# Performance work log

Hardware: AMD Instinct MI355X
Metric: run time of the kernel (lower is better)

## Reference

```python
import jax, jax.numpy as jnp
import numpy as np

N_NODES = 100000
N_EDGES = 1200000
NODE_IN = 64
EDGE_IN = 32
HIDDEN = 64


def _glorot(key, shape):
    fan_in, fan_out = shape[0], shape[1]
    s = jnp.sqrt(2.0 / (fan_in + fan_out))
    return jax.random.normal(key, shape, dtype=jnp.float32) * s


def setup_inputs() -> dict:
    key = jax.random.key(0)
    ks = jax.random.split(key, 16)
    inp = {
        "x": jax.random.normal(ks[0], (N_NODES, NODE_IN), dtype=jnp.float32),
        "edge_index": jax.random.randint(ks[1], (2, N_EDGES), 0, N_NODES, dtype=jnp.int64),
        "edge_attr": jax.random.normal(ks[2], (N_EDGES, EDGE_IN), dtype=jnp.float32),
        # SAGE layer 0 (in=NODE_IN -> HIDDEN): lin_l (neighbors, has bias), lin_r (root)
        "w_l0": _glorot(ks[3], (NODE_IN, HIDDEN)),
        "w_r0": _glorot(ks[4], (NODE_IN, HIDDEN)),
        "b0": jnp.zeros((HIDDEN,), jnp.float32),
        "ln_g0": jnp.ones((HIDDEN,), jnp.float32),
        "ln_b0": jnp.zeros((HIDDEN,), jnp.float32),
        # SAGE layer 1 (HIDDEN -> HIDDEN)
        "w_l1": _glorot(ks[5], (HIDDEN, HIDDEN)),
        "w_r1": _glorot(ks[6], (HIDDEN, HIDDEN)),
        "b1": jnp.zeros((HIDDEN,), jnp.float32),
        "ln_g1": jnp.ones((HIDDEN,), jnp.float32),
        "ln_b1": jnp.zeros((HIDDEN,), jnp.float32),
        # Edge classifier MLP: in_dim = 3*HIDDEN + EDGE_IN = 224
        "cw1": _glorot(ks[7], (3 * HIDDEN + EDGE_IN, HIDDEN)),
        "cb1": jnp.zeros((HIDDEN,), jnp.float32),
        "cw2": _glorot(ks[8], (HIDDEN, HIDDEN // 2)),
        "cb2": jnp.zeros((HIDDEN // 2,), jnp.float32),
        "cw3": _glorot(ks[9], (HIDDEN // 2, 1)),
        "cb3": jnp.zeros((1,), jnp.float32),
    }
    return inp


def _sage_conv(x, src, dst, w_l, w_r, b):
    # mean-aggregate source features at destination nodes (PyG SAGEConv, aggr='mean')
    n = x.shape[0]
    msg = x[src]  # [E, F] gather
    agg = jax.ops.segment_sum(msg, dst, num_segments=n)
    cnt = jax.ops.segment_sum(jnp.ones((src.shape[0], 1), x.dtype), dst, num_segments=n)
    mean = agg / jnp.maximum(cnt, 1.0)
    return mean @ w_l + x @ w_r + b


def _layer_norm(x, g, b, eps=1e-5):
    mu = jnp.mean(x, axis=-1, keepdims=True)
    var = jnp.var(x, axis=-1, keepdims=True)
    return (x - mu) * jax.lax.rsqrt(var + eps) * g + b


def reference(x, edge_index, edge_attr,
              w_l0, w_r0, b0, ln_g0, ln_b0,
              w_l1, w_r1, b1, ln_g1, ln_b1,
              cw1, cb1, cw2, cb2, cw3, cb3):
    src, dst = edge_index[0], edge_index[1]
    # Encoder (eval mode: dropout is identity)
    h = jax.nn.relu(_layer_norm(_sage_conv(x, src, dst, w_l0, w_r0, b0), ln_g0, ln_b0))
    z = jax.nn.relu(_layer_norm(_sage_conv(h, src, dst, w_l1, w_r1, b1), ln_g1, ln_b1))
    # Edge classifier: gather-concat-MLP
    z_src = z[src]
    z_dst = z[dst]
    edge_repr = jnp.concatenate([z_src, z_dst, z_src * z_dst, edge_attr], axis=-1)
    h1 = jax.nn.relu(edge_repr @ cw1 + cb1)
    h2 = jax.nn.relu(h1 @ cw2 + cb2)
    logits = (h2 @ cw3 + cb3).squeeze(-1)  # [E]
    return logits
```

## Files before the change

kernel.cpp:

```cpp
#include <hip/hip_runtime.h>
#include <hip/hip_bf16.h>

#define N_NODES 100000
#define N_EDGES 1200000

typedef __attribute__((ext_vector_type(8))) short bfrag;
typedef __attribute__((ext_vector_type(4))) float ffrag;

union FragU { uint4 v; uint32_t u[4]; bfrag f; };

__device__ __forceinline__ float rl_f(float v, int k) {
  return __int_as_float(__builtin_amdgcn_readlane(__float_as_int(v), k));
}
__device__ __forceinline__ int rl_i(int v, int k) {
  return __builtin_amdgcn_readlane(v, k);
}
__device__ __forceinline__ ushort bfbits(float a) {
  union { __hip_bfloat16 h; ushort u; } c; c.h = __float2bfloat16(a); return c.u;
}
__device__ __forceinline__ uint32_t pkbf(float a, float b) {
  union { __hip_bfloat162 h; uint32_t u; } c;
  c.h = __float22bfloat162_rn(float2{a, b}); return c.u;
}
__device__ __forceinline__ uint32_t mul2bf(uint32_t a, uint32_t b) {
  union { uint32_t u; __hip_bfloat162 h; } x, y, r;
  x.u = a; y.u = b; r.h = __hmul2(x.h, y.h); return r.u;
}
__device__ __forceinline__ float bflo(uint32_t u) { return __int_as_float(u << 16); }
__device__ __forceinline__ float bfhi(uint32_t u) { return __int_as_float(u & 0xffff0000u); }


__global__ void cvt_k(const float* __restrict__ x, ushort* __restrict__ xb, int n2) {
  int i = blockIdx.x * blockDim.x + threadIdx.x;
  if (i < n2) {
    float2 v = ((const float2*)x)[i];
    ((uint32_t*)xb)[i] = pkbf(v.x, v.y);
  }
}


__global__ void hist_k(const int* __restrict__ ei, int* __restrict__ deg, int E) {
  int e = blockIdx.x * blockDim.x + threadIdx.x;
  if (e < E) atomicAdd(&deg[ei[E + e]], 1);
}

__global__ __launch_bounds__(1024) void scan1_k(const int* __restrict__ deg,
                                                int* __restrict__ off,
                                                int* __restrict__ bsum, int n) {
  __shared__ int wpart[16];
  __shared__ int wpre[16];
  int tid = threadIdx.x, lane = tid & 63, wid = tid >> 6;
  int i = blockIdx.x * 1024 + tid;
  int v = (i < n) ? deg[i] : 0;
  int x = v;
  #pragma unroll
  for (int o = 1; o < 64; o <<= 1) {
    int y = __shfl_up(x, o);
    if (lane >= o) x += y;
  }
  if (lane == 63) wpart[wid] = x;
  __syncthreads();
  if (tid == 0) {
    int run = 0;
    #pragma unroll
    for (int w = 0; w < 16; w++) { int t = wpart[w]; wpre[w] = run; run += t; }
    bsum[blockIdx.x] = run;
  }
  __syncthreads();
  if (i < n) off[i] = x - v + wpre[wid];
}

__global__ void scan2_k(const int* __restrict__ bsum, int* __restrict__ bpre,
                        int* __restrict__ off, int nb, int n) {
  if (threadIdx.x == 0) {
    int run = 0;
    for (int b = 0; b < nb; b++) { int t = bsum[b]; bpre[b] = run; run += t; }
    off[n] = run;
  }
}

__global__ __launch_bounds__(1024) void scan3_k(int* __restrict__ off, int* __restrict__ pos,
                                                const int* __restrict__ bpre, int n) {
  int i = blockIdx.x * 1024 + threadIdx.x;
  if (i < n) {
    int o = off[i] + bpre[blockIdx.x];
    off[i] = o;
    pos[i] = o;
  }
}

__global__ void fill_k(const int* __restrict__ ei, int* __restrict__ pos,
                       int* __restrict__ csr, int E) {
  int e = blockIdx.x * blockDim.x + threadIdx.x;
  if (e < E) {
    int d = ei[E + e];
    int p = atomicAdd(&pos[d], 1);
    csr[p] = ei[e];
  }
}


__global__ __launch_bounds__(256) void agg_k(
    const ushort* __restrict__ Xb, const int* __restrict__ off, const int* __restrict__ csr,
    ushort* __restrict__ aggout, int n) {
  int lane = threadIdx.x & 63;
  int half = lane >> 5, f2 = lane & 31;
  int wave = blockIdx.x * 4 + (threadIdx.x >> 6);
  int nw = gridDim.x * 4;
  for (int i = wave; i < n; i += nw) {
    int s0 = off[i], s1 = off[i + 1];
    float a0 = 0.f, a1 = 0.f;
    for (int base = s0; base < s1; base += 64) {
      int rem = s1 - base;
      int cnt = rem < 64 ? rem : 64;
      int myidx = (lane < cnt) ? csr[base + lane] : 0;
      int j = 0;
      for (; j + 8 <= cnt; j += 8) {
        uint32_t us[4];
        #pragma unroll
        for (int p = 0; p < 4; p++) {
          int i0 = rl_i(myidx, j + 2 * p), i1 = rl_i(myidx, j + 2 * p + 1);
          int sel = half ? i1 : i0;
          us[p] = ((const uint32_t*)Xb)[(size_t)sel * 32 + f2];
        }
        #pragma unroll
        for (int p = 0; p < 4; p++) { a0 += bflo(us[p]); a1 += bfhi(us[p]); }
      }
      for (; j + 2 <= cnt; j += 2) {
        int i0 = rl_i(myidx, j), i1 = rl_i(myidx, j + 1);
        int sel = half ? i1 : i0;
        uint32_t u = ((const uint32_t*)Xb)[(size_t)sel * 32 + f2];
        a0 += bflo(u); a1 += bfhi(u);
      }
      if (j < cnt) {
        int i0 = rl_i(myidx, j);
        uint32_t u = ((const uint32_t*)Xb)[(size_t)i0 * 32 + f2];
        if (half == 0) { a0 += bflo(u); a1 += bfhi(u); }
      }
    }
    a0 += __shfl_xor(a0, 32);
    a1 += __shfl_xor(a1, 32);
    int d = s1 - s0;
    float rdeg = 1.f / fmaxf((float)d, 1.f);
    if (half == 0)
      ((uint32_t*)aggout)[(size_t)i * 32 + f2] = pkbf(a0 * rdeg, a1 * rdeg);
  }
}


__global__ __launch_bounds__(256) void node_k(
    const ushort* __restrict__ agg, const ushort* __restrict__ selfb,
    const float* __restrict__ wl, const float* __restrict__ wr,
    const float* __restrict__ bias, const float* __restrict__ g, const float* __restrict__ lb,
    ushort* __restrict__ outb, int n) {
  __shared__ ushort wt[64 * 128];
  const int tid = threadIdx.x;
  for (int i = tid; i < 8192; i += 256) {
    int k = i >> 6, nn = i & 63;
    float v = (k < 64) ? wl[k * 64 + nn] : wr[(k - 64) * 64 + nn];
    wt[nn * 128 + (((k >> 3) ^ (nn & 7)) * 8) + (k & 7)] = bfbits(v);
  }
  __syncthreads();
  const int lane = tid & 63, wid = tid >> 6;
  const int ln = lane & 15, q = lane >> 4;
  float bias_n[4], g_n[4], lb_n[4];
  #pragma unroll
  for (int nt = 0; nt < 4; nt++) {
    bias_n[nt] = bias[nt * 16 + ln];
    g_n[nt] = g[nt * 16 + ln];
    lb_n[nt] = lb[nt * 16 + ln];
  }
  const int ntiles = (n + 15) >> 4;
  for (int t = blockIdx.x * 4 + wid; t < ntiles; t += gridDim.x * 4) {
    int node = t * 16 + ln;
    int nc = node < n ? node : n - 1;
    FragU afr[4];
    #pragma unroll
    for (int kk = 0; kk < 2; kk++) {
      afr[kk].v     = ((const uint4*)agg)[(size_t)nc * 8 + kk * 4 + q];
      afr[2 + kk].v = ((const uint4*)selfb)[(size_t)nc * 8 + kk * 4 + q];
    }
    ffrag acc[4];
    #pragma unroll
    for (int nt = 0; nt < 4; nt++) acc[nt] = ffrag{0.f, 0.f, 0.f, 0.f};
    #pragma unroll
    for (int kk = 0; kk < 4; kk++) {
      bfrag a = afr[kk].f;
      #pragma unroll
      for (int nt = 0; nt < 4; nt++) {
        int nn = nt * 16 + ln;
        int b = kk * 4 + q;
        const bfrag* bp = (const bfrag*)&wt[nn * 128 + ((b ^ (nn & 7)) * 8)];
        acc[nt] = __builtin_amdgcn_mfma_f32_16x16x32_bf16(a, *bp, acc[nt], 0, 0, 0);
      }
    }
    #pragma unroll
    for (int r = 0; r < 4; r++) {
      int m = t * 16 + q * 4 + r;
      float o[4];
      #pragma unroll
      for (int nt = 0; nt < 4; nt++) o[nt] = acc[nt][r] + bias_n[nt];
      float s = (o[0] + o[1]) + (o[2] + o[3]);
      #pragma unroll
      for (int mm = 1; mm < 16; mm <<= 1) s += __shfl_xor(s, mm);
      float mu = s * (1.f / 64.f);
      float v2 = 0.f;
      #pragma unroll
      for (int nt = 0; nt < 4; nt++) { float d2 = o[nt] - mu; v2 += d2 * d2; }
      #pragma unroll
      for (int mm = 1; mm < 16; mm <<= 1) v2 += __shfl_xor(v2, mm);
      float rs = rsqrtf(v2 * (1.f / 64.f) + 1e-5f);
      if (m < n) {
        #pragma unroll
        for (int nt = 0; nt < 4; nt++) {
          float y = fmaxf((o[nt] - mu) * rs * g_n[nt] + lb_n[nt], 0.f);
          outb[(size_t)m * 64 + nt * 16 + ln] = bfbits(y);
        }
      }
    }
  }
}


__global__ __launch_bounds__(256) void edge_mfma_k(
    const int* __restrict__ ei, const float* __restrict__ ea,
    const ushort* __restrict__ zb,
    const float* __restrict__ cw1, const float* __restrict__ cb1,
    const float* __restrict__ cw2, const float* __restrict__ cb2,
    const float* __restrict__ cw3, const float* __restrict__ cb3,
    float* __restrict__ out, int E) {
  __shared__ ushort wt1[64 * 256];
  __shared__ ushort h1b[4][16 * 64];
  const int tid = threadIdx.x;

  for (int i = tid; i < 224 * 64; i += 256) {
    int k = i >> 6, n = i & 63;
    int blk = k >> 3;
    wt1[n * 256 + ((blk ^ (n & 7)) * 8) + (k & 7)] = bfbits(cw1[i]);
  }
  __syncthreads();

  const int lane = tid & 63, wid = tid >> 6;
  const int ln = lane & 15, q = lane >> 4;

  float cb1v[4];
  #pragma unroll
  for (int t = 0; t < 4; t++) cb1v[t] = cb1[t * 16 + ln];
  float cb2a = cb2[ln], cb2b = cb2[16 + ln];
  float w3a = cw3[ln], w3b = cw3[16 + ln];
  float cb3v = cb3[0];

  FragU w2f[2][2];
  #pragma unroll
  for (int t2 = 0; t2 < 2; t2++) {
    #pragma unroll
    for (int kk = 0; kk < 2; kk++) {
      #pragma unroll
      for (int p = 0; p < 4; p++) {
        int k = kk * 32 + q * 8 + p * 2;
        int n = t2 * 16 + ln;
        w2f[t2][kk].u[p] = pkbf(cw2[k * 32 + n], cw2[(k + 1) * 32 + n]);
      }
    }
  }

  ushort* hb = h1b[wid];
  const int ntiles = E >> 4;
  for (int t = blockIdx.x * 4 + wid; t < ntiles; t += gridDim.x * 4) {
    int e = t * 16 + ln;
    int s = ei[e], d = ei[E + e];

    FragU afr[7];
    #pragma unroll
    for (int kk = 0; kk < 2; kk++) {
      afr[kk].v     = ((const uint4*)zb)[(size_t)s * 8 + kk * 4 + q];
      afr[2 + kk].v = ((const uint4*)zb)[(size_t)d * 8 + kk * 4 + q];
    }
    #pragma unroll
    for (int kk = 0; kk < 2; kk++) {
      #pragma unroll
      for (int p = 0; p < 4; p++)
        afr[4 + kk].u[p] = mul2bf(afr[kk].u[p], afr[2 + kk].u[p]);
    }
    {
      float4 lo = ((const float4*)ea)[(size_t)e * 8 + q * 2];
      float4 hi = ((const float4*)ea)[(size_t)e * 8 + q * 2 + 1];
      afr[6].u[0] = pkbf(lo.x, lo.y); afr[6].u[1] = pkbf(lo.z, lo.w);
      afr[6].u[2] = pkbf(hi.x, hi.y); afr[6].u[3] = pkbf(hi.z, hi.w);
    }

    ffrag acc1[4];
    #pragma unroll
    for (int tt = 0; tt < 4; tt++) acc1[tt] = ffrag{0.f, 0.f, 0.f, 0.f};

    #pragma unroll
    for (int kk = 0; kk < 7; kk++) {
      bfrag a = afr[kk].f;
      #pragma unroll
      for (int tt = 0; tt < 4; tt++) {
        int n = tt * 16 + ln;
        int b = kk * 4 + q;
        const bfrag* bp = (const bfrag*)&wt1[n * 256 + ((b ^ (n & 7)) * 8)];
        acc1[tt] = __builtin_amdgcn_mfma_f32_16x16x32_bf16(a, *bp, acc1[tt], 0, 0, 0);
      }
    }

    #pragma unroll
    for (int tt = 0; tt < 4; tt++) {
      #pragma unroll
      for (int r = 0; r < 4; r++) {
        int m = q * 4 + r;
        int col = tt * 16 + ln;
        float v = fmaxf(acc1[tt][r] + cb1v[tt], 0.f);
        hb[m * 64 + (((col >> 3) ^ (m & 7)) * 8) + (col & 7)] = bfbits(v);
      }
    }

    ffrag acc2[2];
    acc2[0] = ffrag{0.f, 0.f, 0.f, 0.f};
    acc2[1] = ffrag{0.f, 0.f, 0.f, 0.f};
    #pragma unroll
    for (int kk = 0; kk < 2; kk++) {
      int b = kk * 4 + q;
      const bfrag* ap = (const bfrag*)&hb[ln * 64 + ((b ^ (ln & 7)) * 8)];
      bfrag a2 = *ap;
      acc2[0] = __builtin_amdgcn_mfma_f32_16x16x32_bf16(a2, w2f[0][kk].f, acc2[0], 0, 0, 0);
      acc2[1] = __builtin_amdgcn_mfma_f32_16x16x32_bf16(a2, w2f[1][kk].f, acc2[1], 0, 0, 0);
    }

    float p0, p1, p2, p3;
    {
      p0 = fmaxf(acc2[0][0] + cb2a, 0.f) * w3a + fmaxf(acc2[1][0] + cb2b, 0.f) * w3b;
      p1 = fmaxf(acc2[0][1] + cb2a, 0.f) * w3a + fmaxf(acc2[1][1] + cb2b, 0.f) * w3b;
      p2 = fmaxf(acc2[0][2] + cb2a, 0.f) * w3a + fmaxf(acc2[1][2] + cb2b, 0.f) * w3b;
      p3 = fmaxf(acc2[0][3] + cb2a, 0.f) * w3a + fmaxf(acc2[1][3] + cb2b, 0.f) * w3b;
    }
    #pragma unroll
    for (int o = 1; o < 16; o <<= 1) {
      p0 += __shfl_xor(p0, o);
      p1 += __shfl_xor(p1, o);
      p2 += __shfl_xor(p2, o);
      p3 += __shfl_xor(p3, o);
    }
    float keep = (ln == 0) ? p0 : (ln == 1) ? p1 : (ln == 2) ? p2 : p3;
    if (ln < 4) out[t * 16 + q * 4 + ln] = keep + cb3v;
  }
}


extern "C" void kernel_launch(void* const* d_in, const int* in_sizes, int n_in,
                              void* d_out, int out_size, void* d_ws, size_t ws_size,
                              hipStream_t stream) {
  const float* x   = (const float*)d_in[0];
  const int*   ei  = (const int*)d_in[1];
  const float* ea  = (const float*)d_in[2];
  const float* wl0 = (const float*)d_in[3];
  const float* wr0 = (const float*)d_in[4];
  const float* b0  = (const float*)d_in[5];
  const float* g0  = (const float*)d_in[6];
  const float* lb0 = (const float*)d_in[7];
  const float* wl1 = (const float*)d_in[8];
  const float* wr1 = (const float*)d_in[9];
  const float* b1  = (const float*)d_in[10];
  const float* g1  = (const float*)d_in[11];
  const float* lb1 = (const float*)d_in[12];
  const float* cw1 = (const float*)d_in[13];
  const float* cb1 = (const float*)d_in[14];
  const float* cw2 = (const float*)d_in[15];
  const float* cb2 = (const float*)d_in[16];
  const float* cw3 = (const float*)d_in[17];
  const float* cb3 = (const float*)d_in[18];
  float* out = (float*)d_out;
  const int N = N_NODES, E = N_EDGES;
  const int NB = (N + 1023) / 1024;

  uintptr_t pp = (uintptr_t)d_ws;
  auto alloc = [&](size_t bytes) {
    uintptr_t r = (pp + 255) & ~(uintptr_t)255; pp = r + bytes; return (void*)r;
  };
  int* deg  = (int*)alloc((size_t)N * 4);
  int* off  = (int*)alloc((size_t)(N + 1) * 4);
  int* pos  = (int*)alloc((size_t)N * 4);
  int* csr  = (int*)alloc((size_t)E * 4);
  int* bsum = (int*)alloc((size_t)NB * 4);
  int* bpre = (int*)alloc((size_t)NB * 4);
  ushort* xb  = (ushort*)alloc((size_t)N * 64 * 2);
  ushort* agg = (ushort*)alloc((size_t)N * 64 * 2);
  ushort* hb  = (ushort*)alloc((size_t)N * 64 * 2);
  ushort* zb  = (ushort*)alloc((size_t)N * 64 * 2);

  hipMemsetAsync(deg, 0, (size_t)N * 4, stream);
  cvt_k<<<(N * 32 + 255) / 256, 256, 0, stream>>>(x, xb, N * 32);
  hist_k<<<(E + 255) / 256, 256, 0, stream>>>(ei, deg, E);
  scan1_k<<<NB, 1024, 0, stream>>>(deg, off, bsum, N);
  scan2_k<<<1, 64, 0, stream>>>(bsum, bpre, off, NB, N);
  scan3_k<<<NB, 1024, 0, stream>>>(off, pos, bpre, N);
  fill_k<<<(E + 255) / 256, 256, 0, stream>>>(ei, pos, csr, E);
  agg_k<<<2048, 256, 0, stream>>>(xb, off, csr, agg, N);
  node_k<<<512, 256, 0, stream>>>(agg, xb, wl0, wr0, b0, g0, lb0, hb, N);
  agg_k<<<2048, 256, 0, stream>>>(hb, off, csr, agg, N);
  node_k<<<512, 256, 0, stream>>>(agg, hb, wl1, wr1, b1, g1, lb1, zb, N);
  edge_mfma_k<<<1024, 256, 0, stream>>>(ei, ea, zb, cw1, cb1, cw2, cb2, cw3, cb3, out, E);
}
```

Baseline: 584.7 us.

## Aggregate four nodes per wave and keep edge MLP weights in registers

The aggregation kernel now gives each 16-lane quarter of a wave its own node. Each lane loads 8 bytes of the feature row and unrolls eight neighbour gathers, replacing the readlane-broadcast scheme that used one wave per node. The edge classifier no longer stages the first-layer weights in LDS. Each lane holds its 7x4 bf16 B-fragments in registers, launch bounds are set for occupancy 2, and the grid is halved. This removes the LDS fill and the LDS reads per MFMA, but raises register pressure, and low-degree nodes waste lanes on padded gathers.

New measurement: 561.2 us. -4.0%, faster.

```diff
diff --git a/kernel.cpp b/kernel.cpp
--- a/kernel.cpp
+++ b/kernel.cpp
@@ -9,12 +9,6 @@
 
 union FragU { uint4 v; uint32_t u[4]; bfrag f; };
 
-__device__ __forceinline__ float rl_f(float v, int k) {
-  return __int_as_float(__builtin_amdgcn_readlane(__float_as_int(v), k));
-}
-__device__ __forceinline__ int rl_i(int v, int k) {
-  return __builtin_amdgcn_readlane(v, k);
-}
 __device__ __forceinline__ ushort bfbits(float a) {
   union { __hip_bfloat16 h; ushort u; } c; c.h = __float2bfloat16(a); return c.u;
 }
@@ -104,46 +98,40 @@
     const ushort* __restrict__ Xb, const int* __restrict__ off, const int* __restrict__ csr,
     ushort* __restrict__ aggout, int n) {
   int lane = threadIdx.x & 63;
-  int half = lane >> 5, f2 = lane & 31;
+  int quad = lane >> 4, f8 = lane & 15;
   int wave = blockIdx.x * 4 + (threadIdx.x >> 6);
   int nw = gridDim.x * 4;
-  for (int i = wave; i < n; i += nw) {
-    int s0 = off[i], s1 = off[i + 1];
-    float a0 = 0.f, a1 = 0.f;
-    for (int base = s0; base < s1; base += 64) {
-      int rem = s1 - base;
-      int cnt = rem < 64 ? rem : 64;
-      int myidx = (lane < cnt) ? csr[base + lane] : 0;
-      int j = 0;
-      for (; j + 8 <= cnt; j += 8) {
-        uint32_t us[4];
-        #pragma unroll
-        for (int p = 0; p < 4; p++) {
-          int i0 = rl_i(myidx, j + 2 * p), i1 = rl_i(myidx, j + 2 * p + 1);
-          int sel = half ? i1 : i0;
-          us[p] = ((const uint32_t*)Xb)[(size_t)sel * 32 + f2];
+  int nquads = (n + 3) >> 2;
+  const uint2* X2 = (const uint2*)Xb;
+  for (int p = wave; p < nquads; p += nw) {
+    int i = p * 4 + quad;
+    int ic = i < n ? i : n - 1;
+    int s0 = off[ic], s1 = off[ic + 1];
+    float a0 = 0.f, a1 = 0.f, a2 = 0.f, a3 = 0.f;
+    for (int j = s0; j < s1; j += 8) {
+      int id[8]; uint2 us[8];
+      #pragma unroll
+      for (int u = 0; u < 8; u++) {
+        int jj = j + u;
+        id[u] = csr[jj < s1 ? jj : s1 - 1];
+      }
+      #pragma unroll
+      for (int u = 0; u < 8; u++) us[u] = X2[(size_t)id[u] * 16 + f8];
+      #pragma unroll
+      for (int u = 0; u < 8; u++) {
+        if (j + u < s1) {
+          a0 += bflo(us[u].x); a1 += bfhi(us[u].x);
+          a2 += bflo(us[u].y); a3 += bfhi(us[u].y);
         }
-        #pragma unroll
-        for (int p = 0; p < 4; p++) { a0 += bflo(us[p]); a1 += bfhi(us[p]); }
-      }
-      for (; j + 2 <= cnt; j += 2) {
-        int i0 = rl_i(myidx, j), i1 = rl_i(myidx, j + 1);
-        int sel = half ? i1 : i0;
-        uint32_t u = ((const uint32_t*)Xb)[(size_t)sel * 32 + f2];
-        a0 += bflo(u); a1 += bfhi(u);
-      }
-      if (j < cnt) {
-        int i0 = rl_i(myidx, j);
-        uint32_t u = ((const uint32_t*)Xb)[(size_t)i0 * 32 + f2];
-        if (half == 0) { a0 += bflo(u); a1 += bfhi(u); }
-      }
-    }
-    a0 += __shfl_xor(a0, 32);
-    a1 += __shfl_xor(a1, 32);
-    int d = s1 - s0;
-    float rdeg = 1.f / fmaxf((float)d, 1.f);
-    if (half == 0)
-      ((uint32_t*)aggout)[(size_t)i * 32 + f2] = pkbf(a0 * rdeg, a1 * rdeg);
+      }
+    }
+    if (i < n) {
+      float rdeg = 1.f / fmaxf((float)(s1 - s0), 1.f);
+      uint2 w;
+      w.x = pkbf(a0 * rdeg, a1 * rdeg);
+      w.y = pkbf(a2 * rdeg, a3 * rdeg);
+      ((uint2*)aggout)[(size_t)i * 16 + f8] = w;
+    }
   }
 }
 
@@ -222,26 +210,44 @@
 }
 
 
-__global__ __launch_bounds__(256) void edge_mfma_k(
+__global__ __launch_bounds__(256, 2) void edge_mfma_k(
     const int* __restrict__ ei, const float* __restrict__ ea,
     const ushort* __restrict__ zb,
     const float* __restrict__ cw1, const float* __restrict__ cb1,
     const float* __restrict__ cw2, const float* __restrict__ cb2,
     const float* __restrict__ cw3, const float* __restrict__ cb3,
     float* __restrict__ out, int E) {
-  __shared__ ushort wt1[64 * 256];
   __shared__ ushort h1b[4][16 * 64];
   const int tid = threadIdx.x;
-
-  for (int i = tid; i < 224 * 64; i += 256) {
-    int k = i >> 6, n = i & 63;
-    int blk = k >> 3;
-    wt1[n * 256 + ((blk ^ (n & 7)) * 8) + (k & 7)] = bfbits(cw1[i]);
-  }
-  __syncthreads();
-
   const int lane = tid & 63, wid = tid >> 6;
   const int ln = lane & 15, q = lane >> 4;
+
+  FragU w1f[7][4];
+  #pragma unroll
+  for (int kk = 0; kk < 7; kk++) {
+    #pragma unroll
+    for (int tt = 0; tt < 4; tt++) {
+      #pragma unroll
+      for (int p = 0; p < 4; p++) {
+        int k = (kk * 4 + q) * 8 + p * 2;
+        int n = tt * 16 + ln;
+        w1f[kk][tt].u[p] = pkbf(cw1[k * 64 + n], cw1[(k + 1) * 64 + n]);
+      }
+    }
+  }
+  FragU w2f[2][2];
+  #pragma unroll
+  for (int t2 = 0; t2 < 2; t2++) {
+    #pragma unroll
+    for (int kk = 0; kk < 2; kk++) {
+      #pragma unroll
+      for (int p = 0; p < 4; p++) {
+        int k = kk * 32 + q * 8 + p * 2;
+        int n = t2 * 16 + ln;
+        w2f[t2][kk].u[p] = pkbf(cw2[k * 32 + n], cw2[(k + 1) * 32 + n]);
+      }
+    }
+  }
 
   float cb1v[4];
   #pragma unroll
@@ -249,20 +255,6 @@
   float cb2a = cb2[ln], cb2b = cb2[16 + ln];
   float w3a = cw3[ln], w3b = cw3[16 + ln];
   float cb3v = cb3[0];
-
-  FragU w2f[2][2];
-  #pragma unroll
-  for (int t2 = 0; t2 < 2; t2++) {
-    #pragma unroll
-    for (int kk = 0; kk < 2; kk++) {
-      #pragma unroll
-      for (int p = 0; p < 4; p++) {
-        int k = kk * 32 + q * 8 + p * 2;
-        int n = t2 * 16 + ln;
-        w2f[t2][kk].u[p] = pkbf(cw2[k * 32 + n], cw2[(k + 1) * 32 + n]);
-      }
-    }
-  }
 
   ushort* hb = h1b[wid];
   const int ntiles = E >> 4;
@@ -276,33 +268,28 @@
       afr[kk].v     = ((const uint4*)zb)[(size_t)s * 8 + kk * 4 + q];
       afr[2 + kk].v = ((const uint4*)zb)[(size_t)d * 8 + kk * 4 + q];
     }
-    #pragma unroll
-    for (int kk = 0; kk < 2; kk++) {
-      #pragma unroll
-      for (int p = 0; p < 4; p++)
-        afr[4 + kk].u[p] = mul2bf(afr[kk].u[p], afr[2 + kk].u[p]);
-    }
     {
       float4 lo = ((const float4*)ea)[(size_t)e * 8 + q * 2];
       float4 hi = ((const float4*)ea)[(size_t)e * 8 + q * 2 + 1];
       afr[6].u[0] = pkbf(lo.x, lo.y); afr[6].u[1] = pkbf(lo.z, lo.w);
       afr[6].u[2] = pkbf(hi.x, hi.y); afr[6].u[3] = pkbf(hi.z, hi.w);
     }
+    #pragma unroll
+    for (int kk = 0; kk < 2; kk++) {
+      #pragma unroll
+      for (int p = 0; p < 4; p++)
+        afr[4 + kk].u[p] = mul2bf(afr[kk].u[p], afr[2 + kk].u[p]);
+    }
 
     ffrag acc1[4];
     #pragma unroll
     for (int tt = 0; tt < 4; tt++) acc1[tt] = ffrag{0.f, 0.f, 0.f, 0.f};
-
     #pragma unroll
     for (int kk = 0; kk < 7; kk++) {
       bfrag a = afr[kk].f;
       #pragma unroll
-      for (int tt = 0; tt < 4; tt++) {
-        int n = tt * 16 + ln;
-        int b = kk * 4 + q;
-        const bfrag* bp = (const bfrag*)&wt1[n * 256 + ((b ^ (n & 7)) * 8)];
-        acc1[tt] = __builtin_amdgcn_mfma_f32_16x16x32_bf16(a, *bp, acc1[tt], 0, 0, 0);
-      }
+      for (int tt = 0; tt < 4; tt++)
+        acc1[tt] = __builtin_amdgcn_mfma_f32_16x16x32_bf16(a, w1f[kk][tt].f, acc1[tt], 0, 0, 0);
     }
 
     #pragma unroll
@@ -400,5 +387,5 @@
   node_k<<<512, 256, 0, stream>>>(agg, xb, wl0, wr0, b0, g0, lb0, hb, N);
   agg_k<<<2048, 256, 0, stream>>>(hb, off, csr, agg, N);
   node_k<<<512, 256, 0, stream>>>(agg, hb, wl1, wr1, b1, g1, lb1, zb, N);
-  edge_mfma_k<<<1024, 256, 0, stream>>>(ei, ea, zb, cw1, cb1, cw2, cb2, cw3, cb3, out, E);
-}
+  edge_mfma_k<<<512, 256, 0, stream>>>(ei, ea, zb, cw1, cb1, cw2, cb2, cw3, cb3, out, E);
+}
```
